# Kernel tuning notes

Measured on AMD Instinct MI355X. Metric: run time of the kernel, lower is better.

## Reference

```python
import jax, jax.numpy as jnp
import numpy as np

EPS = 1e-5

def setup_inputs() -> dict:
    key = jax.random.key(0)
    k1, k2, k3, k4 = jax.random.split(key, 4)
    Cin, Cout, K = 128, 256, 3
    x = jax.random.normal(k1, (32, Cin, 56, 56), dtype=jnp.float32)
    # kaiming_normal fan_in relu: std = sqrt(2 / (Cin*K*K))
    std = np.sqrt(2.0 / (Cin * K * K)).astype(np.float32)
    weight = jax.random.normal(k2, (Cout, Cin, K, K), dtype=jnp.float32) * std
    bias = jnp.zeros((Cout,), dtype=jnp.float32)
    gamma = jnp.ones((Cout,), dtype=jnp.float32)
    beta = jnp.zeros((Cout,), dtype=jnp.float32)
    return {"x": x, "weight": weight, "bias": bias, "gamma": gamma, "beta": beta}

def reference(x, weight, bias, gamma, beta):
    # conv2d, stride=1, padding=1 (NCHW, OIHW)
    y = jax.lax.conv_general_dilated(
        x, weight, window_strides=(1, 1), padding=((1, 1), (1, 1)),
        dimension_numbers=("NCHW", "OIHW", "NCHW"))
    y = y + bias[None, :, None, None]
    # BatchNorm2d, training mode: batch stats over (N,H,W), biased variance
    mean = jnp.mean(y, axis=(0, 2, 3), keepdims=True)
    var = jnp.mean(jnp.square(y - mean), axis=(0, 2, 3), keepdims=True)
    y = (y - mean) * jax.lax.rsqrt(var + EPS)
    y = y * gamma[None, :, None, None] + beta[None, :, None, None]
    return jax.nn.relu(y)
```

## Files before the change

### kernel.cpp

```cpp
#include <hip/hip_runtime.h>
#include <hip/hip_bf16.h>

typedef short v8s __attribute__((ext_vector_type(8)));
typedef float f32x4 __attribute__((ext_vector_type(4)));
typedef unsigned short u16;
typedef unsigned int u32;

#define HW_   3136
#define W_    56
#define PW_   58
#define CIN_  128
#define COUT_ 256
#define NB_   32
#define KCNT  100352.0f

#define XP_ELEMS (NB_*PW_*PW_*CIN_)
#define WT_ELEMS (9*COUT_*CIN_)
#define WT_OFFB  (XP_ELEMS*2)
#define ST_OFFB  (WT_OFFB + WT_ELEMS*2)

#define PAD_BLOCKS (NB_*PW_)
#define WT_BLOCKS  (WT_ELEMS/256)

#define GLOAD16(g, l) __builtin_amdgcn_global_load_lds( \
    (const __attribute__((address_space(1))) u32*)(g), \
    (__attribute__((address_space(3))) u32*)(l), 16, 0, 0)

extern "C" __global__ void __launch_bounds__(256)
pre_kernel(const float* __restrict__ x, const float* __restrict__ wgt,
           u16* __restrict__ xp, u16* __restrict__ wt, float* __restrict__ stats)
{
    const int b   = blockIdx.x;
    const int tid = threadIdx.x;

    if (b >= PAD_BLOCKS) {
        const int e   = (b - PAD_BLOCKS) * 256 + tid;
        const int ci  = e & 127;
        const int t2  = e >> 7;
        const int co  = t2 & 255;
        const int tap = t2 >> 8;
        __hip_bfloat16 bv = __float2bfloat16(wgt[co * 1152 + ci * 9 + tap]);
        wt[e] = *(u16*)&bv;
        if (b == PAD_BLOCKS) {
            stats[tid] = 0.f;
            stats[tid + 256] = 0.f;
        }
        return;
    }

    const int n  = b / PW_;
    const int hp = b - n * PW_;
    u16* rowp = xp + (n * PW_ + hp) * PW_ * CIN_;

    if (hp == 0 || hp == PW_ - 1) {
        #pragma unroll
        for (int k = 0; k < 4; ++k) {
            const int j = tid + k * 256;
            if (j < PW_ * CIN_ / 8)
                *(v8s*)&rowp[j * 8] = (v8s){0,0,0,0,0,0,0,0};
        }
        return;
    }

    __shared__ float tile[CIN_ * 58];
    const float* xrow = x + n * CIN_ * HW_ + (hp - 1) * W_;
    for (int idx = tid; idx < CIN_ * 14; idx += 256) {
        const int c  = idx / 14;
        const int w4 = idx - c * 14;
        const float4 v = *(const float4*)&xrow[c * HW_ + w4 * 4];
        float* tp = &tile[c * 58 + w4 * 4];
        tp[0] = v.x; tp[1] = v.y; tp[2] = v.z; tp[3] = v.w;
    }
    __syncthreads();

    if (tid < 32) {
        const int wp = (tid >> 4) * (PW_ - 1);
        const int cg = tid & 15;
        *(v8s*)&rowp[wp * CIN_ + cg * 8] = (v8s){0,0,0,0,0,0,0,0};
    }
    for (int idx = tid; idx < W_ * 16; idx += 256) {
        const int wp = (idx >> 4) + 1;
        const int cg = idx & 15;
        v8s v;
        #pragma unroll
        for (int j = 0; j < 8; ++j) {
            __hip_bfloat16 bv = __float2bfloat16(tile[(cg * 8 + j) * 58 + (wp - 1)]);
            v[j] = *(short*)&bv;
        }
        *(v8s*)&rowp[wp * CIN_ + cg * 8] = v;
    }
}

extern "C" __global__ void __launch_bounds__(256)
conv_kernel(const u16* __restrict__ xp, const u16* __restrict__ wt,
            const float* __restrict__ bias, float* __restrict__ out,
            float* __restrict__ stats)
{
    __shared__ u16 As[2 * 128 * 64];
    __shared__ u16 Bs[2 * 128 * 64];

    const int t    = threadIdx.x;
    const int lane = t & 63;
    const int wid  = t >> 6;

    const int bid     = blockIdx.x;
    const int logical = (bid & 7) * 196 + (bid >> 3);
    const int cbase   = (logical & 1) << 7;
    const int mbase   = (logical >> 1) << 7;

    const int srow8 = lane >> 3;
    const int swz   = ((lane & 7) ^ srow8) << 3;
    int xa[4], wb[4];
    #pragma unroll
    for (int i = 0; i < 4; ++i) {
        const int r   = wid * 32 + i * 8 + srow8;
        const int m   = mbase + r;
        const int n0  = m / HW_;
        const int hw0 = m - n0 * HW_;
        const int h0  = hw0 / W_;
        const int w0  = hw0 - h0 * W_;
        xa[i] = ((n0 * PW_ + h0) * PW_ + w0) * CIN_ + swz;
        wb[i] = (cbase + r) * CIN_ + swz;
    }

    f32x4 acc[4][4];
    #pragma unroll
    for (int i = 0; i < 4; ++i)
        #pragma unroll
        for (int j = 0; j < 4; ++j) acc[i][j] = (f32x4){0.f, 0.f, 0.f, 0.f};

    const int wr = wid >> 1, wc = wid & 1;
    const int frow = lane & 15;
    const int kg   = lane >> 4;

    #pragma unroll
    for (int i = 0; i < 4; ++i) {
        GLOAD16(xp + xa[i], As + (wid * 32 + i * 8) * 64);
        GLOAD16(wt + wb[i], Bs + (wid * 32 + i * 8) * 64);
    }
    __syncthreads();

    #pragma unroll 1
    for (int kt = 0; kt < 18; ++kt) {
        const int cur = kt & 1;
        const u16* acur = As + cur * 8192;
        const u16* bcur = Bs + cur * 8192;

        if (kt < 17) {
            const int ktn  = kt + 1;
            const int tap  = ktn >> 1;
            const int kh   = (tap * 11) >> 5;
            const int kw   = tap - kh * 3;
            const int xoff = (kh * PW_ + kw) * CIN_ + ((ktn & 1) << 6);
            const int woff = tap * (COUT_ * CIN_) + ((ktn & 1) << 6);
            u16* apre = As + (cur ^ 1) * 8192;
            u16* bpre = Bs + (cur ^ 1) * 8192;
            #pragma unroll
            for (int i = 0; i < 4; ++i) {
                GLOAD16(xp + xa[i] + xoff, apre + (wid * 32 + i * 8) * 64);
                GLOAD16(wt + wb[i] + woff, bpre + (wid * 32 + i * 8) * 64);
            }
        }

        #pragma unroll
        for (int ks = 0; ks < 2; ++ks) {
            const int ck = (((ks << 2) | kg) ^ (frow & 7)) << 3;
            v8s af[4], bf4[4];
            #pragma unroll
            for (int mf = 0; mf < 4; ++mf)
                af[mf] = *(const v8s*)(acur + (wr * 64 + mf * 16 + frow) * 64 + ck);
            #pragma unroll
            for (int nf = 0; nf < 4; ++nf)
                bf4[nf] = *(const v8s*)(bcur + (wc * 64 + nf * 16 + frow) * 64 + ck);
            #pragma unroll
            for (int mf = 0; mf < 4; ++mf)
                #pragma unroll
                for (int nf = 0; nf < 4; ++nf)
                    acc[mf][nf] = __builtin_amdgcn_mfma_f32_16x16x32_bf16(
                        af[mf], bf4[nf], acc[mf][nf], 0, 0, 0);
        }

        __syncthreads();
    }

    const int lgrp = lane >> 4;
    #pragma unroll
    for (int nf = 0; nf < 4; ++nf) {
        const int co = cbase + wc * 64 + nf * 16 + frow;
        const float bv = bias[co];
        float s = 0.f, q = 0.f;
        #pragma unroll
        for (int mf = 0; mf < 4; ++mf) {
            const int mloc = wr * 64 + mf * 16 + lgrp * 4;
            const int mg2  = mbase + mloc;
            const int n2   = mg2 / HW_;
            const int hw2  = mg2 - n2 * HW_;
            float4 ov; float vx;
            vx = acc[mf][nf][0] + bv; ov.x = vx; s += vx; q += vx * vx;
            vx = acc[mf][nf][1] + bv; ov.y = vx; s += vx; q += vx * vx;
            vx = acc[mf][nf][2] + bv; ov.z = vx; s += vx; q += vx * vx;
            vx = acc[mf][nf][3] + bv; ov.w = vx; s += vx; q += vx * vx;
            *(float4*)(out + (n2 * COUT_ + co) * HW_ + hw2) = ov;
        }
        s += __shfl_xor(s, 16); s += __shfl_xor(s, 32);
        q += __shfl_xor(q, 16); q += __shfl_xor(q, 32);
        if (lgrp == 0) {
            atomicAdd(&stats[co], s);
            atomicAdd(&stats[COUT_ + co], q);
        }
    }
}

extern "C" __global__ void bn_kernel(float* __restrict__ y, const float* __restrict__ stats,
                                     const float* __restrict__ gamma, const float* __restrict__ beta)
{
    const int i4 = blockIdx.x * 256 + threadIdx.x;
    const int e  = i4 * 4;
    const int co = (e / HW_) & (COUT_ - 1);
    const float inv  = 1.f / KCNT;
    const float mean = stats[co] * inv;
    const float var  = stats[COUT_ + co] * inv - mean * mean;
    const float scale = gamma[co] * rsqrtf(var + 1e-5f);
    const float shift = beta[co] - mean * scale;
    float4 v = *(float4*)(y + e);
    v.x = fmaxf(fmaf(v.x, scale, shift), 0.f);
    v.y = fmaxf(fmaf(v.y, scale, shift), 0.f);
    v.z = fmaxf(fmaf(v.z, scale, shift), 0.f);
    v.w = fmaxf(fmaf(v.w, scale, shift), 0.f);
    *(float4*)(y + e) = v;
}

extern "C" void kernel_launch(void* const* d_in, const int* in_sizes, int n_in,
                              void* d_out, int out_size, void* d_ws, size_t ws_size,
                              hipStream_t stream)
{
    const float* x     = (const float*)d_in[0];
    const float* wgt   = (const float*)d_in[1];
    const float* bias  = (const float*)d_in[2];
    const float* gamma = (const float*)d_in[3];
    const float* beta  = (const float*)d_in[4];
    float* out = (float*)d_out;

    char* ws = (char*)d_ws;
    u16*   xp    = (u16*)ws;
    u16*   wt    = (u16*)(ws + WT_OFFB);
    float* stats = (float*)(ws + ST_OFFB);

    pre_kernel<<<PAD_BLOCKS + WT_BLOCKS, 256, 0, stream>>>(x, wgt, xp, wt, stats);
    conv_kernel<<<1568, 256, 0, stream>>>(xp, wt, bias, out, stats);
    bn_kernel<<<(out_size / 4) / 256, 256, 0, stream>>>(out, stats, gamma, beta);
}
```

Measured before the change: 273.7 us.

## Enlarge conv tile to 256x256 with 8 waves and restructured double-buffer pipeline

```diff
diff --git a/kernel.cpp b/kernel.cpp
--- a/kernel.cpp
+++ b/kernel.cpp
@@ -91,107 +91,118 @@
     }
 }
 
-extern "C" __global__ void __launch_bounds__(256)
+#define STAGE(P, XOFF, WOFF) {                                                 \
+    u16* ap_ = As + (P) * 16384;                                               \
+    u16* bp_ = Bs + (P) * 16384;                                               \
+    _Pragma("unroll")                                                          \
+    for (int i_ = 0; i_ < 4; ++i_) {                                           \
+        GLOAD16(xp + xa[i_] + (XOFF), ap_ + (i_ * 64 + wid * 8) * 64);         \
+        GLOAD16(wt + wb[i_] + (WOFF), bp_ + (i_ * 64 + wid * 8) * 64);         \
+    } }
+
+#define ITER(P, STG, XOFF, WOFF) {                                             \
+    const u16* ab_ = As + (P) * 16384;                                         \
+    const u16* bb_ = Bs + (P) * 16384;                                         \
+    v8s af_[8], bf_[4];                                                        \
+    _Pragma("unroll")                                                          \
+    for (int mf = 0; mf < 8; ++mf) af_[mf] = *(const v8s*)(ab_ + arow[mf] + ck0); \
+    _Pragma("unroll")                                                          \
+    for (int nf = 0; nf < 4; ++nf) bf_[nf] = *(const v8s*)(bb_ + brow[nf] + ck0); \
+    _Pragma("unroll")                                                          \
+    for (int mf = 0; mf < 8; ++mf)                                             \
+        _Pragma("unroll")                                                      \
+        for (int nf = 0; nf < 4; ++nf)                                         \
+            acc[mf][nf] = __builtin_amdgcn_mfma_f32_16x16x32_bf16(             \
+                af_[mf], bf_[nf], acc[mf][nf], 0, 0, 0);                       \
+    v8s ag_[8], bg_[4];                                                        \
+    _Pragma("unroll")                                                          \
+    for (int mf = 0; mf < 8; ++mf) ag_[mf] = *(const v8s*)(ab_ + arow[mf] + ck1); \
+    _Pragma("unroll")                                                          \
+    for (int nf = 0; nf < 4; ++nf) bg_[nf] = *(const v8s*)(bb_ + brow[nf] + ck1); \
+    __syncthreads();               \
+    if (STG) { STAGE(P, XOFF, WOFF) }                                          \
+    _Pragma("unroll")                                                          \
+    for (int mf = 0; mf < 8; ++mf)                                             \
+        _Pragma("unroll")                                                      \
+        for (int nf = 0; nf < 4; ++nf)                                         \
+            acc[mf][nf] = __builtin_amdgcn_mfma_f32_16x16x32_bf16(             \
+                ag_[mf], bg_[nf], acc[mf][nf], 0, 0, 0);                       \
+    __syncthreads();               \
+}
+
+extern "C" __global__ void __launch_bounds__(512, 2)
 conv_kernel(const u16* __restrict__ xp, const u16* __restrict__ wt,
             const float* __restrict__ bias, float* __restrict__ out,
             float* __restrict__ stats)
 {
-    __shared__ u16 As[2 * 128 * 64];
-    __shared__ u16 Bs[2 * 128 * 64];
+    __shared__ u16 As[2 * 16384];
+    __shared__ u16 Bs[2 * 16384];
 
     const int t    = threadIdx.x;
     const int lane = t & 63;
     const int wid  = t >> 6;
 
-    const int bid     = blockIdx.x;
-    const int logical = (bid & 7) * 196 + (bid >> 3);
-    const int cbase   = (logical & 1) << 7;
-    const int mbase   = (logical >> 1) << 7;
-
-    const int srow8 = lane >> 3;
-    const int swz   = ((lane & 7) ^ srow8) << 3;
+    const int bid   = blockIdx.x;
+    const int mbase = ((bid & 7) * 49 + (bid >> 3)) << 8;
+
+    const int srow = lane >> 3;
+    const int swzc = ((lane & 7) ^ srow) << 3;
     int xa[4], wb[4];
     #pragma unroll
     for (int i = 0; i < 4; ++i) {
-        const int r   = wid * 32 + i * 8 + srow8;
+        const int r   = i * 64 + wid * 8 + srow;
         const int m   = mbase + r;
         const int n0  = m / HW_;
         const int hw0 = m - n0 * HW_;
         const int h0  = hw0 / W_;
         const int w0  = hw0 - h0 * W_;
-        xa[i] = ((n0 * PW_ + h0) * PW_ + w0) * CIN_ + swz;
-        wb[i] = (cbase + r) * CIN_ + swz;
-    }
-
-    f32x4 acc[4][4];
-    #pragma unroll
-    for (int i = 0; i < 4; ++i)
-        #pragma unroll
-        for (int j = 0; j < 4; ++j) acc[i][j] = (f32x4){0.f, 0.f, 0.f, 0.f};
-
-    const int wr = wid >> 1, wc = wid & 1;
+        xa[i] = ((n0 * PW_ + h0) * PW_ + w0) * CIN_ + swzc;
+        wb[i] = r * CIN_ + swzc;
+    }
+
+    const int wr = wid >> 2, wc = wid & 3;
     const int frow = lane & 15;
     const int kg   = lane >> 4;
-
-    #pragma unroll
-    for (int i = 0; i < 4; ++i) {
-        GLOAD16(xp + xa[i], As + (wid * 32 + i * 8) * 64);
-        GLOAD16(wt + wb[i], Bs + (wid * 32 + i * 8) * 64);
-    }
+    const int ck0  = ((kg)     ^ (frow & 7)) << 3;
+    const int ck1  = ((4 | kg) ^ (frow & 7)) << 3;
+    int arow[8], brow[4];
+    #pragma unroll
+    for (int mf = 0; mf < 8; ++mf) arow[mf] = (wr * 128 + mf * 16 + frow) * 64;
+    #pragma unroll
+    for (int nf = 0; nf < 4; ++nf) brow[nf] = (wc * 64 + nf * 16 + frow) * 64;
+
+    f32x4 acc[8][4];
+    #pragma unroll
+    for (int i = 0; i < 8; ++i)
+        #pragma unroll
+        for (int j = 0; j < 4; ++j) acc[i][j] = (f32x4){0.f, 0.f, 0.f, 0.f};
+
+    STAGE(0, 0, 0);
+    STAGE(1, 64, 64);
     __syncthreads();
 
     #pragma unroll 1
-    for (int kt = 0; kt < 18; ++kt) {
-        const int cur = kt & 1;
-        const u16* acur = As + cur * 8192;
-        const u16* bcur = Bs + cur * 8192;
-
-        if (kt < 17) {
-            const int ktn  = kt + 1;
-            const int tap  = ktn >> 1;
-            const int kh   = (tap * 11) >> 5;
-            const int kw   = tap - kh * 3;
-            const int xoff = (kh * PW_ + kw) * CIN_ + ((ktn & 1) << 6);
-            const int woff = tap * (COUT_ * CIN_) + ((ktn & 1) << 6);
-            u16* apre = As + (cur ^ 1) * 8192;
-            u16* bpre = Bs + (cur ^ 1) * 8192;
-            #pragma unroll
-            for (int i = 0; i < 4; ++i) {
-                GLOAD16(xp + xa[i] + xoff, apre + (wid * 32 + i * 8) * 64);
-                GLOAD16(wt + wb[i] + woff, bpre + (wid * 32 + i * 8) * 64);
-            }
-        }
-
-        #pragma unroll
-        for (int ks = 0; ks < 2; ++ks) {
-            const int ck = (((ks << 2) | kg) ^ (frow & 7)) << 3;
-            v8s af[4], bf4[4];
-            #pragma unroll
-            for (int mf = 0; mf < 4; ++mf)
-                af[mf] = *(const v8s*)(acur + (wr * 64 + mf * 16 + frow) * 64 + ck);
-            #pragma unroll
-            for (int nf = 0; nf < 4; ++nf)
-                bf4[nf] = *(const v8s*)(bcur + (wc * 64 + nf * 16 + frow) * 64 + ck);
-            #pragma unroll
-            for (int mf = 0; mf < 4; ++mf)
-                #pragma unroll
-                for (int nf = 0; nf < 4; ++nf)
-                    acc[mf][nf] = __builtin_amdgcn_mfma_f32_16x16x32_bf16(
-                        af[mf], bf4[nf], acc[mf][nf], 0, 0, 0);
-        }
-
-        __syncthreads();
-    }
+    for (int tt = 0; tt < 8; ++tt) {
+        const int tap = tt + 1;
+        const int kh  = (tap * 11) >> 5;
+        const int kw  = tap - kh * 3;
+        const int xo  = (kh * PW_ + kw) * CIN_;
+        const int wo  = tap * (COUT_ * CIN_);
+        ITER(0, 1, xo, wo);
+        ITER(1, 1, xo + 64, wo + 64);
+    }
+    ITER(0, 0, 0, 0);
+    ITER(1, 0, 0, 0);
 
     const int lgrp = lane >> 4;
     #pragma unroll
     for (int nf = 0; nf < 4; ++nf) {
-        const int co = cbase + wc * 64 + nf * 16 + frow;
+        const int co = wc * 64 + nf * 16 + frow;
         const float bv = bias[co];
         float s = 0.f, q = 0.f;
         #pragma unroll
-        for (int mf = 0; mf < 4; ++mf) {
-            const int mloc = wr * 64 + mf * 16 + lgrp * 4;
+        for (int mf = 0; mf < 8; ++mf) {
+            const int mloc = wr * 128 + mf * 16 + lgrp * 4;
             const int mg2  = mbase + mloc;
             const int n2   = mg2 / HW_;
             const int hw2  = mg2 - n2 * HW_;
@@ -247,6 +258,6 @@
     float* stats = (float*)(ws + ST_OFFB);
 
     pre_kernel<<<PAD_BLOCKS + WT_BLOCKS, 256, 0, stream>>>(x, wgt, xp, wt, stats);
-    conv_kernel<<<1568, 256, 0, stream>>>(xp, wt, bias, out, stats);
+    conv_kernel<<<392, 512, 0, stream>>>(xp, wt, bias, out, stats);
     bn_kernel<<<(out_size / 4) / 256, 256, 0, stream>>>(out, stats, gamma, beta);
 }
```

Result: faster. 259.9 us (-5.0%).
